# Kernel optimization log

Measured on AMD Instinct MI355X. Metric: run time of the kernel, lower is better.

Reference implementation:

```python
import jax, jax.numpy as jnp
import numpy as np

B, N, H = 8, 128, 512   # batch, num_sent (n == m required by the 'all' branch), hidden_size
D = 2 * H               # bi-LSTM output dim
SCALE = 0.05


def setup_inputs() -> dict:
    key = jax.random.key(0)
    ks = jax.random.split(key, 24)
    p = lambda k, shape: (jax.random.normal(k, shape, dtype=jnp.float32) * SCALE)
    return {
        "x0_enc": jax.random.normal(ks[0], (B, N, D), dtype=jnp.float32),
        "x1_enc": jax.random.normal(ks[1], (B, N, D), dtype=jnp.float32),
        # concat_attention
        "Wc1": p(ks[2], (D, H)), "Wc2": p(ks[3], (D, H)), "vc": p(ks[4], (H,)),
        # bilinear_attention
        "Wb": p(ks[5], (D, D)),
        # dot_attention x2 (separate params)
        "Wd1": p(ks[6], (D, H)), "vd1": p(ks[7], (H,)),
        "Wd2": p(ks[8], (D, H)), "vd2": p(ks[9], (H,)),
        # minus_attention (Ws/vs are unused in forward)
        "Wm": p(ks[10], (D, H)), "vm": p(ks[11], (H,)),
        # aggregation_layer
        "Wq": p(ks[12], (D, H)), "vq": p(ks[13], (H,)),
        "Wp1": p(ks[14], (2 * D, H)), "Wp2": p(ks[15], (D, H)), "vp": p(ks[16], (H,)),
        "Wpred": p(ks[17], (2 * D, 2)), "bpred": jnp.zeros((2,), dtype=jnp.float32),
    }


def _dot_att(x, y, Wd, vd):
    # sjt[b,m,n] = vd . tanh(Wd(x[b,n] * y[b,m]))  -- pairwise elementwise product + MLP
    z = jnp.tanh(jnp.einsum("bnd,bmd,dh->bmnh", x, y, Wd))  # [B,m,n,H]
    s = jnp.einsum("bmnh,h->bmn", z, vd)
    a = jax.nn.softmax(s, axis=2)
    return jnp.einsum("bmn,bnd->bmd", a, x)


def _minus_att(x, y, Wm, vm):
    # Wm is linear, so Wm(x_n - y_m) = (x@Wm)_n - (y@Wm)_m
    a, b = x @ Wm, y @ Wm                                    # [B,n,H], [B,m,H]
    z = jnp.tanh(a[:, None, :, :] - b[:, :, None, :])        # [B,m,n,H]
    s = jnp.einsum("bmnh,h->bmn", z, vm)
    att = jax.nn.softmax(s, axis=2)
    return jnp.einsum("bmn,bnd->bmd", att, x)


def _concat_att(x, y, Wc1, Wc2, vc):
    a, b = x @ Wc1, y @ Wc2                                  # [B,n,H], [B,m,H]
    z = jnp.tanh(a[:, None, :, :] + b[:, :, None, :])        # [B,m,n,H]
    s = jnp.einsum("bmnh,h->bmn", z, vc)
    att = jax.nn.softmax(s, axis=2)
    return jnp.einsum("bmn,bnd->bmd", att, x)


def _bilinear_att(x, y, Wb):
    s = jnp.einsum("bmd,bnd->bmn", y, x @ Wb)
    att = jax.nn.softmax(s, axis=2)
    return jnp.einsum("bmn,bnd->bmd", att, x)


def reference(x0_enc, x1_enc, Wc1, Wc2, vc, Wb, Wd1, vd1, Wd2, vd2, Wm, vm,
              Wq, vq, Wp1, Wp2, vp, Wpred, bpred):
    x0, x1 = x0_enc, x1_enc
    # attention_fx('all')
    qtc = _concat_att(x0, x1, Wc1, Wc2, vc)
    qtb = _bilinear_att(x0, x1, Wb)
    qts = _dot_att(x0, x1, Wd1, vd1)
    qtd = _dot_att(x1, x0, Wd2, vd2)
    qtm = _minus_att(x0, x1, Wm, vm)
    agg_res = jnp.max(jnp.stack([x1, qts, qtc, qtd, qtb, qtm], axis=0), axis=0)  # [B,m,2H]
    # MultiAtt: dropout is identity in eval
    agg_rep = jnp.concatenate([x1, agg_res], axis=2)                             # [B,m,4H]
    # aggregation_layer
    sj = jnp.einsum("bnh,h->bn", jnp.tanh(x0 @ Wq), vq)
    rq = jnp.einsum("bn,bnd->bd", jax.nn.softmax(sj, axis=1), x0)                # [B,2H]
    t = agg_rep @ Wp1 + (rq @ Wp2)[:, None, :]                                   # [B,m,H]
    sp = jax.nn.softmax(jnp.einsum("bmh,h->bm", t, vp), axis=1)
    rp = jnp.einsum("bm,bmd->bd", sp, agg_rep)                                   # [B,4H]
    out = jax.nn.relu(rp @ Wpred + bpred)                                        # [B,2]
    return out
```

## Files before the change

### kernel.cpp

```cpp
#include <hip/hip_runtime.h>
#include <hip/hip_bf16.h>

static constexpr int Bc = 8, Nc = 128, Dc = 1024, Hc = 512;
static constexpr int BM = Bc * Nc;

typedef _Float16 half8 __attribute__((ext_vector_type(8)));
typedef __fp16 fp16x2 __attribute__((ext_vector_type(2)));
typedef float floatx4 __attribute__((ext_vector_type(4)));

__device__ __forceinline__ float fast_tanh(float x) {
  x = fminf(fmaxf(x, -15.f), 15.f);
  float e = __expf(2.f * x);
  return (e - 1.f) / (e + 1.f);
}

__device__ __forceinline__ unsigned pkh2(float a, float b) {
  fp16x2 h = __builtin_amdgcn_cvt_pkrtz(a, b);
  return __builtin_bit_cast(unsigned, h);
}

__device__ __forceinline__ ushort f2h(float f) {
  _Float16 h = (_Float16)f;
  return __builtin_bit_cast(ushort, h);
}

__device__ __forceinline__ float block_sum256(float v, float* buf4) {
  #pragma unroll
  for (int o = 32; o; o >>= 1) v += __shfl_down(v, o, 64);
  const int w = threadIdx.x >> 6, lane = threadIdx.x & 63;
  if (lane == 0) buf4[w] = v;
  __syncthreads();
  return buf4[0] + buf4[1] + buf4[2] + buf4[3];
}

__global__ __launch_bounds__(256) void cvt_both(const float* __restrict__ x0,
                                                const float* __restrict__ x1,
                                                ushort* __restrict__ o0,
                                                ushort* __restrict__ o1) {
  int bi = blockIdx.x;
  const float* src = (bi < 512) ? x0 : x1;
  ushort* dst = (bi < 512) ? o0 : o1;
  int off = (bi & 511);
  int i = (off * 256 + threadIdx.x) * 8;
  float4 a = *reinterpret_cast<const float4*>(&src[i]);
  float4 b = *reinterpret_cast<const float4*>(&src[i + 4]);
  uint4 o;
  o.x = pkh2(a.x, a.y); o.y = pkh2(a.z, a.w);
  o.z = pkh2(b.x, b.y); o.w = pkh2(b.z, b.w);
  *reinterpret_cast<uint4*>(&dst[i]) = o;
}

struct TJobs {
  const float* src[7];
  ushort* dst[7];
  int J[7];
};
__global__ __launch_bounds__(256) void conv_transpose_multi(TJobs jobs) {
  const int job = blockIdx.z;
  const int J = jobs.J[job];
  const int h0 = blockIdx.y * 64;
  if (h0 >= J) return;
  const float* W = jobs.src[job];
  ushort* WT = jobs.dst[job];
  __shared__ float tile[64][65];
  const int d0 = blockIdx.x * 64;
  const int tid = threadIdx.x;
  #pragma unroll
  for (int i = 0; i < 16; i++) {
    int idx = tid + i * 256;
    int dd = idx >> 6, hh = idx & 63;
    tile[dd][hh] = W[(size_t)(d0 + dd) * J + h0 + hh];
  }
  __syncthreads();
  #pragma unroll
  for (int i = 0; i < 16; i++) {
    int idx = tid + i * 256;
    int hh = idx >> 6, dd = idx & 63;
    WT[(size_t)(h0 + hh) * Dc + d0 + dd] = f2h(tile[dd][hh]);
  }
}

__global__ __launch_bounds__(256) void gemm_bt(const ushort* __restrict__ A,
                                               const ushort* __restrict__ BT,
                                               float* __restrict__ Cf,
                                               ushort* __restrict__ Ch,
                                               int K, int ldc,
                                               size_t sA, size_t sB, size_t sC) {
  const int bz = blockIdx.z;
  A  += (size_t)bz * sA;
  BT += (size_t)bz * sB;
  const int m0 = blockIdx.y * 64, n0 = blockIdx.x * 64;
  __shared__ __align__(16) ushort Asl[64][40];
  __shared__ __align__(16) ushort Bsl[64][40];
  const int tid = threadIdx.x, wave = tid >> 6, lane = tid & 63;
  const int quad = lane >> 4, l15 = lane & 15;
  const int wr = (wave & 1) * 32, wc = (wave >> 1) * 32;
  const int rSt = tid >> 2, kSt8 = (tid & 3) * 8;
  floatx4 acc[2][2];
  #pragma unroll
  for (int i = 0; i < 2; i++)
    #pragma unroll
    for (int j = 0; j < 2; j++) acc[i][j] = (floatx4){0.f, 0.f, 0.f, 0.f};
  uint4 pa = *reinterpret_cast<const uint4*>(&A[(size_t)(m0 + rSt) * K + kSt8]);
  uint4 pb = *reinterpret_cast<const uint4*>(&BT[(size_t)(n0 + rSt) * K + kSt8]);
  for (int k0 = 0; k0 < K; k0 += 32) {
    *reinterpret_cast<uint4*>(&Asl[rSt][kSt8]) = pa;
    *reinterpret_cast<uint4*>(&Bsl[rSt][kSt8]) = pb;
    __syncthreads();
    if (k0 + 32 < K) {
      pa = *reinterpret_cast<const uint4*>(&A[(size_t)(m0 + rSt) * K + k0 + 32 + kSt8]);
      pb = *reinterpret_cast<const uint4*>(&BT[(size_t)(n0 + rSt) * K + k0 + 32 + kSt8]);
    }
    half8 af[2], bb[2];
    #pragma unroll
    for (int i = 0; i < 2; i++)
      af[i] = *reinterpret_cast<const half8*>(&Asl[wr + i * 16 + l15][quad * 8]);
    #pragma unroll
    for (int j = 0; j < 2; j++)
      bb[j] = *reinterpret_cast<const half8*>(&Bsl[wc + j * 16 + l15][quad * 8]);
    #pragma unroll
    for (int i = 0; i < 2; i++)
      #pragma unroll
      for (int j = 0; j < 2; j++)
        acc[i][j] = __builtin_amdgcn_mfma_f32_16x16x32_f16(af[i], bb[j], acc[i][j], 0, 0, 0);
    __syncthreads();
  }
  if (Ch) {
    #pragma unroll
    for (int i = 0; i < 2; i++)
      #pragma unroll
      for (int j = 0; j < 2; j++)
        #pragma unroll
        for (int r = 0; r < 4; r++) {
          int row = m0 + wr + i * 16 + quad * 4 + r;
          int col = n0 + wc + j * 16 + l15;
          Ch[(size_t)bz * sC + (size_t)row * ldc + col] = f2h(acc[i][j][r]);
        }
  } else {
    #pragma unroll
    for (int i = 0; i < 2; i++)
      #pragma unroll
      for (int j = 0; j < 2; j++)
        #pragma unroll
        for (int r = 0; r < 4; r++) {
          int row = m0 + wr + i * 16 + quad * 4 + r;
          int col = n0 + wc + j * 16 + l15;
          Cf[(size_t)bz * sC + (size_t)row * ldc + col] = acc[i][j][r];
        }
  }
}

__global__ __launch_bounds__(256, 2) void dot_scores_mfma6(const ushort* __restrict__ X0h,
                                                           const ushort* __restrict__ X1h,
                                                           const ushort* __restrict__ WdT1,
                                                           const ushort* __restrict__ WdT2,
                                                           const float* __restrict__ vd1,
                                                           const float* __restrict__ vd2,
                                                           float* __restrict__ Sd) {
  const int which = blockIdx.z;
  const ushort* Xh = which ? X1h : X0h;
  const ushort* Yh = which ? X0h : X1h;
  const ushort* WdT = which ? WdT2 : WdT1;
  const float* v = which ? vd2 : vd1;
  float* S = Sd + (size_t)which * (BM * Nc);

  const int bm = blockIdx.y;
  const int b = bm >> 7;
  const int hBase = blockIdx.x * 256;
  const int tid = threadIdx.x;
  const int wave = tid >> 6, lane = tid & 63;
  const int quad = lane >> 4, l15 = lane & 15;
  const int wn = wave & 1, wh = wave >> 1;

  __shared__ __align__(16) char smraw[51200];
  ushort (*As0)[32] = (ushort(*)[32])(smraw);
  ushort (*As1)[32] = (ushort(*)[32])(smraw + 8192);
  ushort (*Bs0)[32] = (ushort(*)[32])(smraw + 16384);
  ushort (*Bs1)[32] = (ushort(*)[32])(smraw + 32768);
  ushort* ylh = (ushort*)(smraw + 49152);
  float (*red)[33] = (float(*)[33])(smraw);

  {
    const uint* Yrow = (const uint*)(Yh + (size_t)bm * Dc);
    uint* dst = (uint*)ylh;
    #pragma unroll
    for (int i = 0; i < 2; i++) dst[tid + i * 256] = Yrow[tid + i * 256];
  }

  floatx4 acc[4][8];
  #pragma unroll
  for (int i = 0; i < 4; i++)
    #pragma unroll
    for (int j = 0; j < 8; j++) acc[i][j] = (floatx4){0.f, 0.f, 0.f, 0.f};

  const ushort* Xb = Xh + (size_t)b * Nc * Dc;
  const int nSt = tid >> 2;
  const int kSt8 = (tid & 3) * 8;

  auto stage = [&](int k0, ushort (*Asb)[32], ushort (*Bsb)[32]) {
    half8 yv = *reinterpret_cast<const half8*>(&ylh[k0 + kSt8]);
    #pragma unroll
    for (int p = 0; p < 2; p++) {
      const int n = p * 64 + nSt;
      half8 xv = *reinterpret_cast<const half8*>(&Xb[(size_t)n * Dc + k0 + kSt8]);
      half8 prod = xv * yv;
      *reinterpret_cast<half8*>(&Asb[n][kSt8]) = prod;
    }
    #pragma unroll
    for (int r = 0; r < 4; r++)
      *reinterpret_cast<uint4*>(&Bsb[r * 64 + nSt][kSt8]) =
          *reinterpret_cast<const uint4*>(&WdT[(size_t)(hBase + r * 64 + nSt) * Dc + k0 + kSt8]);
  };

  auto mfma_step = [&](ushort (*Asb)[32], ushort (*Bsb)[32]) {
    half8 af[4], bfr[8];
    #pragma unroll
    for (int i = 0; i < 4; i++)
      af[i] = *reinterpret_cast<const half8*>(&Asb[wn * 64 + i * 16 + l15][quad * 8]);
    #pragma unroll
    for (int j = 0; j < 8; j++)
      bfr[j] = *reinterpret_cast<const half8*>(&Bsb[wh * 128 + j * 16 + l15][quad * 8]);
    #pragma unroll
    for (int i = 0; i < 4; i++)
      #pragma unroll
      for (int j = 0; j < 8; j++)
        acc[i][j] = __builtin_amdgcn_mfma_f32_16x16x32_f16(af[i], bfr[j], acc[i][j], 0, 0, 0);
  };

  __syncthreads();
  stage(0, As0, Bs0);
  __syncthreads();
  #pragma unroll 1
  for (int s = 0; s < 32; s += 2) {
    if (s + 1 < 32) stage((s + 1) * 32, As1, Bs1);
    mfma_step(As0, Bs0);
    __syncthreads();
    if (s + 2 < 32) stage((s + 2) * 32, As0, Bs0);
    mfma_step(As1, Bs1);
    __syncthreads();
  }

  float vv[8];
  #pragma unroll
  for (int j = 0; j < 8; j++) vv[j] = v[hBase + wh * 128 + j * 16 + l15];
  #pragma unroll
  for (int i = 0; i < 4; i++)
    #pragma unroll
    for (int r = 0; r < 4; r++) {
      float p = 0.f;
      #pragma unroll
      for (int j = 0; j < 8; j++) p = fmaf(vv[j], fast_tanh(acc[i][j][r]), p);
      red[wn * 64 + i * 16 + quad * 4 + r][wh * 16 + l15] = p;
    }
  __syncthreads();
  if (tid < 128) {
    float s = 0.f;
    #pragma unroll
    for (int c = 0; c < 32; c++) s += red[tid][c];
    atomicAdd(&S[(size_t)bm * Nc + tid], s);
  }
}

__global__ __launch_bounds__(256) void addtanh_tiled2(const float* __restrict__ C1,
                                                      const float* __restrict__ C2,
                                                      const float* __restrict__ vc,
                                                      const float* __restrict__ vm,
                                                      float* __restrict__ Sc,
                                                      float* __restrict__ Sm) {
  const int nt = blockIdx.x, mt = blockIdx.y;
  const int which = blockIdx.z >> 3, b = blockIdx.z & 7;
  const float* Arow = C1 + which * 512;
  const float* Brow = C2 + which * 512;
  const float* v = which ? vm : vc;
  const float sign = which ? -1.f : 1.f;
  float* S = which ? Sm : Sc;
  __shared__ __align__(16) float at[16][516];
  __shared__ __align__(16) float bt2[16][516];
  __shared__ __align__(16) float vl[512];
  const int tid = threadIdx.x;
  #pragma unroll
  for (int p = 0; p < 8; p++) {
    int idx = p * 256 + tid;
    int r = idx >> 7, c4 = (idx & 127) * 4;
    *reinterpret_cast<float4*>(&at[r][c4]) =
        *reinterpret_cast<const float4*>(&Arow[(size_t)(b * Nc + nt * 16 + r) * 1024 + c4]);
    *reinterpret_cast<float4*>(&bt2[r][c4]) =
        *reinterpret_cast<const float4*>(&Brow[(size_t)(b * Nc + mt * 16 + r) * 1024 + c4]);
  }
  if (tid < 128)
    *reinterpret_cast<float4*>(&vl[tid * 4]) = *reinterpret_cast<const float4*>(&v[tid * 4]);
  __syncthreads();
  const int m = tid >> 4, n = tid & 15;
  float acc = 0.f;
  #pragma unroll 4
  for (int c = 0; c < 512; c += 4) {
    float4 av = *reinterpret_cast<const float4*>(&at[n][c]);
    float4 bv = *reinterpret_cast<const float4*>(&bt2[m][c]);
    float4 vv = *reinterpret_cast<const float4*>(&vl[c]);
    acc = fmaf(vv.x, fast_tanh(fmaf(sign, bv.x, av.x)), acc);
    acc = fmaf(vv.y, fast_tanh(fmaf(sign, bv.y, av.y)), acc);
    acc = fmaf(vv.z, fast_tanh(fmaf(sign, bv.z, av.z)), acc);
    acc = fmaf(vv.w, fast_tanh(fmaf(sign, bv.w, av.w)), acc);
  }
  S[(size_t)(b * Nc + mt * 16 + m) * Nc + nt * 16 + n] = acc;
}

__global__ __launch_bounds__(128) void softmax128(float* __restrict__ S) {
  const int row = blockIdx.x;
  const int tid = threadIdx.x;
  float x = S[(size_t)row * 128 + tid];
  __shared__ float mbuf[2], sbuf[2];
  float mx = x;
  #pragma unroll
  for (int o = 32; o; o >>= 1) mx = fmaxf(mx, __shfl_down(mx, o, 64));
  if ((tid & 63) == 0) mbuf[tid >> 6] = mx;
  __syncthreads();
  mx = fmaxf(mbuf[0], mbuf[1]);
  float e = __expf(x - mx);
  float sm = e;
  #pragma unroll
  for (int o = 32; o; o >>= 1) sm += __shfl_down(sm, o, 64);
  if ((tid & 63) == 0) sbuf[tid >> 6] = sm;
  __syncthreads();
  sm = sbuf[0] + sbuf[1];
  S[(size_t)row * 128 + tid] = e / sm;
}

#define FMA4(acc, s, v)                  \
  acc.x = fmaf(s, v.x, acc.x);           \
  acc.y = fmaf(s, v.y, acc.y);           \
  acc.z = fmaf(s, v.z, acc.z);           \
  acc.w = fmaf(s, v.w, acc.w)

__global__ __launch_bounds__(256) void agg_max(const float* __restrict__ x0,
                                               const float* __restrict__ x1,
                                               const float* __restrict__ Sc,
                                               const float* __restrict__ Sb,
                                               const float* __restrict__ Sd1,
                                               const float* __restrict__ Sd2,
                                               const float* __restrict__ Sm,
                                               const float* __restrict__ u,
                                               float* __restrict__ agg,
                                               float* __restrict__ score) {
  const int bm = blockIdx.x;
  const int b = bm >> 7;
  const int tid = threadIdx.x;
  __shared__ float w[5][128];
  if (tid < 128) {
    w[0][tid] = Sc[(size_t)bm * Nc + tid];
    w[1][tid] = Sb[(size_t)bm * Nc + tid];
    w[2][tid] = Sd1[(size_t)bm * Nc + tid];
    w[3][tid] = Sd2[(size_t)bm * Nc + tid];
    w[4][tid] = Sm[(size_t)bm * Nc + tid];
  }
  __syncthreads();
  const int d0 = tid * 4;
  float4 qc = {0, 0, 0, 0}, qb = {0, 0, 0, 0}, qs = {0, 0, 0, 0};
  float4 qd = {0, 0, 0, 0}, qm = {0, 0, 0, 0};
  const float* X0b = x0 + (size_t)b * Nc * Dc;
  const float* X1b = x1 + (size_t)b * Nc * Dc;
  for (int n = 0; n < Nc; n++) {
    float4 xv = *reinterpret_cast<const float4*>(&X0b[(size_t)n * Dc + d0]);
    float4 yv = *reinterpret_cast<const float4*>(&X1b[(size_t)n * Dc + d0]);
    float wc = w[0][n], wb = w[1][n], ws = w[2][n], wd = w[3][n], wm = w[4][n];
    FMA4(qc, wc, xv);
    FMA4(qb, wb, xv);
    FMA4(qs, ws, xv);
    FMA4(qd, wd, yv);
    FMA4(qm, wm, xv);
  }
  float4 x1v = *reinterpret_cast<const float4*>(&x1[(size_t)bm * Dc + d0]);
  float4 r;
  r.x = fmaxf(x1v.x, fmaxf(fmaxf(qs.x, qc.x), fmaxf(fmaxf(qd.x, qb.x), qm.x)));
  r.y = fmaxf(x1v.y, fmaxf(fmaxf(qs.y, qc.y), fmaxf(fmaxf(qd.y, qb.y), qm.y)));
  r.z = fmaxf(x1v.z, fmaxf(fmaxf(qs.z, qc.z), fmaxf(fmaxf(qd.z, qb.z), qm.z)));
  r.w = fmaxf(x1v.w, fmaxf(fmaxf(qs.w, qc.w), fmaxf(fmaxf(qd.w, qb.w), qm.w)));
  *reinterpret_cast<float4*>(&agg[(size_t)bm * Dc + d0]) = r;
  float4 u1 = *reinterpret_cast<const float4*>(&u[d0]);
  float4 u2 = *reinterpret_cast<const float4*>(&u[Dc + d0]);
  float p = x1v.x * u1.x + x1v.y * u1.y + x1v.z * u1.z + x1v.w * u1.w +
            r.x * u2.x + r.y * u2.y + r.z * u2.z + r.w * u2.w;
  __shared__ float buf4[4];
  p = block_sum256(p, buf4);
  if (tid == 0) score[bm] = p;
}

__global__ __launch_bounds__(64) void compute_u(const float* __restrict__ Wp1,
                                                const float* __restrict__ vp,
                                                float* __restrict__ u) {
  const int d2 = blockIdx.x;
  const int tid = threadIdx.x;
  float p = 0.f;
  #pragma unroll
  for (int h = tid; h < Hc; h += 64) p = fmaf(Wp1[(size_t)d2 * Hc + h], vp[h], p);
  #pragma unroll
  for (int o = 32; o; o >>= 1) p += __shfl_down(p, o, 64);
  if (tid == 0) u[d2] = p;
}

__global__ __launch_bounds__(256) void final_out(const float* __restrict__ x1,
                                                 const float* __restrict__ agg,
                                                 const float* __restrict__ score,
                                                 const float* __restrict__ Wpred,
                                                 const float* __restrict__ bpred,
                                                 float* __restrict__ out) {
  const int b = blockIdx.x;
  const int tid = threadIdx.x;
  __shared__ float spL[128];
  __shared__ float mbuf[2], sbuf[2];
  if (tid < 128) {
    float x = score[b * Nc + tid];
    float mx = x;
    #pragma unroll
    for (int o = 32; o; o >>= 1) mx = fmaxf(mx, __shfl_down(mx, o, 64));
    if ((tid & 63) == 0) mbuf[tid >> 6] = mx;
  }
  __syncthreads();
  if (tid < 128) {
    float x = score[b * Nc + tid];
    float mx = fmaxf(mbuf[0], mbuf[1]);
    float e = __expf(x - mx);
    float sm = e;
    #pragma unroll
    for (int o = 32; o; o >>= 1) sm += __shfl_down(sm, o, 64);
    if ((tid & 63) == 0) sbuf[tid >> 6] = sm;
    spL[tid] = e;
  }
  __syncthreads();
  const float inv = 1.f / (sbuf[0] + sbuf[1]);
  const int d2 = tid * 8;
  float w0[8], w1[8];
  #pragma unroll
  for (int i = 0; i < 8; i++) {
    w0[i] = Wpred[(size_t)(d2 + i) * 2 + 0];
    w1[i] = Wpred[(size_t)(d2 + i) * 2 + 1];
  }
  const float* src = (d2 < Dc) ? (x1 + (size_t)b * Nc * Dc + d2)
                               : (agg + (size_t)b * Nc * Dc + (d2 - Dc));
  float p0 = 0.f, p1 = 0.f;
  for (int m = 0; m < Nc; m++) {
    float s = spL[m] * inv;
    const float* r = src + (size_t)m * Dc;
    #pragma unroll
    for (int i = 0; i < 8; i++) {
      float sc = s * r[i];
      p0 = fmaf(sc, w0[i], p0);
      p1 = fmaf(sc, w1[i], p1);
    }
  }
  #pragma unroll
  for (int o = 32; o; o >>= 1) {
    p0 += __shfl_down(p0, o, 64);
    p1 += __shfl_down(p1, o, 64);
  }
  __shared__ float r0[4], r1[4];
  const int w = tid >> 6, lane = tid & 63;
  if (lane == 0) { r0[w] = p0; r1[w] = p1; }
  __syncthreads();
  if (tid == 0) {
    float q0 = r0[0] + r0[1] + r0[2] + r0[3] + bpred[0];
    float q1 = r1[0] + r1[1] + r1[2] + r1[3] + bpred[1];
    out[b * 2 + 0] = fmaxf(q0, 0.f);
    out[b * 2 + 1] = fmaxf(q1, 0.f);
  }
}

extern "C" void kernel_launch(void* const* d_in, const int* in_sizes, int n_in,
                              void* d_out, int out_size, void* d_ws, size_t ws_size,
                              hipStream_t stream) {
  const float* x0    = (const float*)d_in[0];
  const float* x1    = (const float*)d_in[1];
  const float* Wc1   = (const float*)d_in[2];
  const float* Wc2   = (const float*)d_in[3];
  const float* vc    = (const float*)d_in[4];
  const float* Wb    = (const float*)d_in[5];
  const float* Wd1   = (const float*)d_in[6];
  const float* vd1   = (const float*)d_in[7];
  const float* Wd2   = (const float*)d_in[8];
  const float* vd2   = (const float*)d_in[9];
  const float* Wm    = (const float*)d_in[10];
  const float* vm    = (const float*)d_in[11];
  const float* Wp1   = (const float*)d_in[14];
  const float* vp    = (const float*)d_in[16];
  const float* Wpred = (const float*)d_in[17];
  const float* bpred = (const float*)d_in[18];
  float* out = (float*)d_out;

  float* ws = (float*)d_ws;
  float* C1     = ws;
  float* C2     = C1 + 1048576;
  float* sc     = C2 + 1048576;
  float* sb     = sc + 131072;
  float* sd1    = sb + 131072;
  float* sd2    = sd1 + 131072;
  float* smv    = sd2 + 131072;
  float* u      = smv + 131072;
  float* score2 = u + 2048;
  ushort* x0h   = (ushort*)(score2 + 1024);
  ushort* x1h   = x0h + 1048576;
  ushort* W1T   = x1h + 1048576;
  ushort* W2T   = W1T + 1048576;
  ushort* WbT   = W2T + 1048576;
  ushort* xWbh  = WbT + 1048576;
  ushort* wdT1  = xWbh + 1048576;
  ushort* wdT2  = wdT1 + 524288;
  float* agg    = C1;

  cvt_both<<<1024, 256, 0, stream>>>(x0, x1, x0h, x1h);
  TJobs tj;
  tj.src[0] = Wd1; tj.dst[0] = wdT1;            tj.J[0] = Hc;
  tj.src[1] = Wd2; tj.dst[1] = wdT2;            tj.J[1] = Hc;
  tj.src[2] = Wc1; tj.dst[2] = W1T;             tj.J[2] = Hc;
  tj.src[3] = Wm;  tj.dst[3] = W1T + 512 * Dc;  tj.J[3] = Hc;
  tj.src[4] = Wc2; tj.dst[4] = W2T;             tj.J[4] = Hc;
  tj.src[5] = Wm;  tj.dst[5] = W2T + 512 * Dc;  tj.J[5] = Hc;
  tj.src[6] = Wb;  tj.dst[6] = WbT;             tj.J[6] = Dc;
  conv_transpose_multi<<<dim3(16, 16, 7), 256, 0, stream>>>(tj);
  compute_u<<<2 * Dc, 64, 0, stream>>>(Wp1, vp, u);

  gemm_bt<<<dim3(16, 16, 1), 256, 0, stream>>>(x0h, W1T, C1, nullptr, Dc, 1024, 0, 0, 0);
  gemm_bt<<<dim3(16, 16, 1), 256, 0, stream>>>(x1h, W2T, C2, nullptr, Dc, 1024, 0, 0, 0);
  gemm_bt<<<dim3(16, 16, 1), 256, 0, stream>>>(x0h, WbT, nullptr, xWbh, Dc, 1024, 0, 0, 0);
  gemm_bt<<<dim3(2, 2, 8), 256, 0, stream>>>(x1h, xWbh, sb, nullptr, Dc, 128,
                                             131072, 131072, 16384);

  addtanh_tiled2<<<dim3(8, 8, 16), 256, 0, stream>>>(C1, C2, vc, vm, sc, smv);

  (void)hipMemsetAsync(sd1, 0, 2 * 131072 * sizeof(float), stream);
  dot_scores_mfma6<<<dim3(2, BM, 2), 256, 0, stream>>>(x0h, x1h, wdT1, wdT2, vd1, vd2, sd1);

  softmax128<<<5 * BM, 128, 0, stream>>>(sc);

  agg_max<<<BM, 256, 0, stream>>>(x0, x1, sc, sb, sd1, sd2, smv, u, agg, score2);

  final_out<<<Bc, 256, 0, stream>>>(x1, agg, score2, Wpred, bpred, out);
}
```

Before: 689.9 us.

## Process two query rows per block in dot-attention scores to share weight tiles

The dot-attention score kernel now uses 512-thread blocks that each handle two y rows (m values) at once. The Wd^T tile staged in shared memory is reused by both row groups, which halves weight traffic per output. Loading also changes from double-buffered shared memory to register prefetch with a single shared buffer and two barriers per k-step. The price is more syncs per iteration, fewer blocks in the grid, and possibly lower occupancy from the larger blocks.

```diff
diff --git a/kernel.cpp b/kernel.cpp
--- a/kernel.cpp
+++ b/kernel.cpp
@@ -150,7 +150,7 @@
   }
 }
 
-__global__ __launch_bounds__(256, 2) void dot_scores_mfma6(const ushort* __restrict__ X0h,
+__global__ __launch_bounds__(512, 2) void dot_scores_mfma7(const ushort* __restrict__ X0h,
                                                            const ushort* __restrict__ X1h,
                                                            const ushort* __restrict__ WdT1,
                                                            const ushort* __restrict__ WdT2,
@@ -164,27 +164,25 @@
   const float* v = which ? vd2 : vd1;
   float* S = Sd + (size_t)which * (BM * Nc);
 
-  const int bm = blockIdx.y;
-  const int b = bm >> 7;
+  const int mp = blockIdx.y;
+  const int b = mp >> 6;
   const int hBase = blockIdx.x * 256;
   const int tid = threadIdx.x;
   const int wave = tid >> 6, lane = tid & 63;
   const int quad = lane >> 4, l15 = lane & 15;
-  const int wn = wave & 1, wh = wave >> 1;
-
-  __shared__ __align__(16) char smraw[51200];
-  ushort (*As0)[32] = (ushort(*)[32])(smraw);
-  ushort (*As1)[32] = (ushort(*)[32])(smraw + 8192);
-  ushort (*Bs0)[32] = (ushort(*)[32])(smraw + 16384);
-  ushort (*Bs1)[32] = (ushort(*)[32])(smraw + 32768);
-  ushort* ylh = (ushort*)(smraw + 49152);
-  float (*red)[33] = (float(*)[33])(smraw);
+  const int mg = wave >> 2, wn = (wave >> 1) & 1, wh = wave & 1;
+
+  __shared__ __align__(16) char smraw[36864];
+  ushort* As = (ushort*)smraw;
+  ushort* Bs = (ushort*)(smraw + 16384);
+  ushort* ylh = (ushort*)(smraw + 32768);
+  float (*red)[33] = (float(*)[33])smraw;
 
   {
-    const uint* Yrow = (const uint*)(Yh + (size_t)bm * Dc);
+    const uint* Y0 = (const uint*)(Yh + (size_t)(mp * 2) * Dc);
     uint* dst = (uint*)ylh;
-    #pragma unroll
-    for (int i = 0; i < 2; i++) dst[tid + i * 256] = Yrow[tid + i * 256];
+    dst[tid] = Y0[tid];
+    dst[tid + 512] = Y0[tid + 512];
   }
 
   floatx4 acc[4][8];
@@ -194,32 +192,33 @@
     for (int j = 0; j < 8; j++) acc[i][j] = (floatx4){0.f, 0.f, 0.f, 0.f};
 
   const ushort* Xb = Xh + (size_t)b * Nc * Dc;
-  const int nSt = tid >> 2;
-  const int kSt8 = (tid & 3) * 8;
-
-  auto stage = [&](int k0, ushort (*Asb)[32], ushort (*Bsb)[32]) {
-    half8 yv = *reinterpret_cast<const half8*>(&ylh[k0 + kSt8]);
-    #pragma unroll
-    for (int p = 0; p < 2; p++) {
-      const int n = p * 64 + nSt;
-      half8 xv = *reinterpret_cast<const half8*>(&Xb[(size_t)n * Dc + k0 + kSt8]);
-      half8 prod = xv * yv;
-      *reinterpret_cast<half8*>(&Asb[n][kSt8]) = prod;
-    }
-    #pragma unroll
-    for (int r = 0; r < 4; r++)
-      *reinterpret_cast<uint4*>(&Bsb[r * 64 + nSt][kSt8]) =
-          *reinterpret_cast<const uint4*>(&WdT[(size_t)(hBase + r * 64 + nSt) * Dc + k0 + kSt8]);
+  const int nA = tid >> 2;
+  const int ch8 = (tid & 3) * 8;
+
+  half8 xv;
+  uint4 bv0, bv1;
+  auto loads = [&](int s) {
+    xv = *reinterpret_cast<const half8*>(Xb + (size_t)nA * Dc + s * 32 + ch8);
+    const ushort* wp = WdT + (size_t)(hBase + nA) * Dc + s * 32 + ch8;
+    bv0 = *reinterpret_cast<const uint4*>(wp);
+    bv1 = *reinterpret_cast<const uint4*>(wp + 128 * Dc);
   };
-
-  auto mfma_step = [&](ushort (*Asb)[32], ushort (*Bsb)[32]) {
+  auto stage = [&](int s) {
+    half8 y0 = *reinterpret_cast<const half8*>(ylh + s * 32 + ch8);
+    half8 y1 = *reinterpret_cast<const half8*>(ylh + 1024 + s * 32 + ch8);
+    *reinterpret_cast<half8*>(As + (size_t)nA * 32 + ch8) = xv * y0;
+    *reinterpret_cast<half8*>(As + 4096 + (size_t)nA * 32 + ch8) = xv * y1;
+    *reinterpret_cast<uint4*>(Bs + (size_t)nA * 32 + ch8) = bv0;
+    *reinterpret_cast<uint4*>(Bs + 4096 + (size_t)nA * 32 + ch8) = bv1;
+  };
+  auto mfma_step = [&]() {
     half8 af[4], bfr[8];
     #pragma unroll
     for (int i = 0; i < 4; i++)
-      af[i] = *reinterpret_cast<const half8*>(&Asb[wn * 64 + i * 16 + l15][quad * 8]);
+      af[i] = *reinterpret_cast<const half8*>(As + mg * 4096 + (wn * 64 + i * 16 + l15) * 32 + quad * 8);
     #pragma unroll
     for (int j = 0; j < 8; j++)
-      bfr[j] = *reinterpret_cast<const half8*>(&Bsb[wh * 128 + j * 16 + l15][quad * 8]);
+      bfr[j] = *reinterpret_cast<const half8*>(Bs + (wh * 128 + j * 16 + l15) * 32 + quad * 8);
     #pragma unroll
     for (int i = 0; i < 4; i++)
       #pragma unroll
@@ -227,16 +226,14 @@
         acc[i][j] = __builtin_amdgcn_mfma_f32_16x16x32_f16(af[i], bfr[j], acc[i][j], 0, 0, 0);
   };
 
-  __syncthreads();
-  stage(0, As0, Bs0);
+  loads(0);
   __syncthreads();
   #pragma unroll 1
-  for (int s = 0; s < 32; s += 2) {
-    if (s + 1 < 32) stage((s + 1) * 32, As1, Bs1);
-    mfma_step(As0, Bs0);
+  for (int s = 0; s < 32; s++) {
+    stage(s);
+    if (s + 1 < 32) loads(s + 1);
     __syncthreads();
-    if (s + 2 < 32) stage((s + 2) * 32, As0, Bs0);
-    mfma_step(As1, Bs1);
+    mfma_step();
     __syncthreads();
   }
 
@@ -250,14 +247,14 @@
       float p = 0.f;
       #pragma unroll
       for (int j = 0; j < 8; j++) p = fmaf(vv[j], fast_tanh(acc[i][j][r]), p);
-      red[wn * 64 + i * 16 + quad * 4 + r][wh * 16 + l15] = p;
+      red[mg * 128 + wn * 64 + i * 16 + quad * 4 + r][wh * 16 + l15] = p;
     }
   __syncthreads();
-  if (tid < 128) {
+  if (tid < 256) {
     float s = 0.f;
     #pragma unroll
     for (int c = 0; c < 32; c++) s += red[tid][c];
-    atomicAdd(&S[(size_t)bm * Nc + tid], s);
+    atomicAdd(&S[(size_t)mp * 256 + tid], s);
   }
 }
 
@@ -527,7 +524,7 @@
   addtanh_tiled2<<<dim3(8, 8, 16), 256, 0, stream>>>(C1, C2, vc, vm, sc, smv);
 
   (void)hipMemsetAsync(sd1, 0, 2 * 131072 * sizeof(float), stream);
-  dot_scores_mfma6<<<dim3(2, BM, 2), 256, 0, stream>>>(x0h, x1h, wdT1, wdT2, vd1, vd2, sd1);
+  dot_scores_mfma7<<<dim3(2, BM / 2, 2), 512, 0, stream>>>(x0h, x1h, wdT1, wdT2, vd1, vd2, sd1);
 
   softmax128<<<5 * BM, 128, 0, stream>>>(sc);
 
```

New measurement: 612.5 us. -11.2%, faster.
